# Performance work log

Measured on AMD Instinct MI355X. Metric: run time of the kernel, lower is better.

The kernel has to match this reference:

```python
import jax, jax.numpy as jnp
import numpy as np

N_NODES = 20000
N_EDGES = 320000
N_GRAPHS = 512
IN_FEATS = 128
HID = 256
RDKIT_IN = 2048
RDK_H1, RDK_H2 = 1024, 512
COMB_H1, COMB_H2 = 1024, 512
N_TASKS = 1
EPS = 1e-5


def _lin(k, fan_in, fan_out):
    return jax.random.normal(k, (fan_in, fan_out), jnp.float32) / np.float32(np.sqrt(fan_in))


def setup_inputs() -> dict:
    key = jax.random.key(0)
    ks = jax.random.split(key, 24)
    inp = {}
    inp["node_feats"] = jax.random.normal(ks[0], (N_NODES, IN_FEATS), jnp.float32)
    inp["rdkit_feats"] = jax.random.normal(ks[1], (N_GRAPHS, RDKIT_IN), jnp.float32)
    inp["src"] = jax.random.randint(ks[2], (N_EDGES,), 0, N_NODES, dtype=jnp.int32)
    inp["dst"] = jax.random.randint(ks[3], (N_EDGES,), 0, N_NODES, dtype=jnp.int32)
    # sorted graph ids; first N_GRAPHS entries guarantee every graph has >=1 node
    gid = jnp.concatenate([jnp.arange(N_GRAPHS, dtype=jnp.int32),
                           jax.random.randint(ks[4], (N_NODES - N_GRAPHS,), 0, N_GRAPHS, dtype=jnp.int32)])
    inp["node_gid"] = jnp.sort(gid)
    # GCN layer params (GraphConv W,b + residual Linear + BatchNorm gamma/beta)
    dims = [(IN_FEATS, HID), (HID, HID)]
    for i, (fi, fo) in enumerate(dims, start=1):
        inp[f"W{i}"] = _lin(ks[4 + 4 * i], fi, fo)
        inp[f"b{i}"] = jnp.zeros((fo,), jnp.float32)
        inp[f"rW{i}"] = _lin(ks[5 + 4 * i], fi, fo)
        inp[f"rb{i}"] = jnp.zeros((fo,), jnp.float32)
        inp[f"g{i}"] = jnp.ones((fo,), jnp.float32)
        inp[f"be{i}"] = jnp.zeros((fo,), jnp.float32)
    inp["aw_W"] = _lin(ks[16], HID, 1)
    inp["aw_b"] = jnp.zeros((1,), jnp.float32)
    inp["rk_W1"] = _lin(ks[17], RDKIT_IN, RDK_H1)
    inp["rk_b1"] = jnp.zeros((RDK_H1,), jnp.float32)
    inp["rk_W2"] = _lin(ks[18], RDK_H1, RDK_H2)
    inp["rk_b2"] = jnp.zeros((RDK_H2,), jnp.float32)
    comb_in = RDK_H2 + 2 * HID
    inp["c_W1"] = _lin(ks[19], comb_in, COMB_H1)
    inp["c_b1"] = jnp.zeros((COMB_H1,), jnp.float32)
    inp["c_W2"] = _lin(ks[20], COMB_H1, COMB_H2)
    inp["c_b2"] = jnp.zeros((COMB_H2,), jnp.float32)
    inp["c_W3"] = _lin(ks[21], COMB_H2, N_TASKS)
    inp["c_b3"] = jnp.zeros((N_TASKS,), jnp.float32)
    return inp


def _gcn_layer(h, src, dst, W, b, rW, rb, g, be):
    # GraphConv, norm='none': sum incoming messages of (X W), then bias + relu
    m = h @ W                                                    # [N, out]
    agg = jax.ops.segment_sum(m[src], dst, num_segments=h.shape[0])
    new = jax.nn.relu(agg + b)
    # residual Linear with activation (dgllife GCNLayer)
    new = new + jax.nn.relu(h @ rW + rb)
    # BatchNorm1d over nodes (training-mode batch stats; dropout in eval = identity)
    mu = new.mean(axis=0)
    var = new.var(axis=0)
    return g * (new - mu) * jax.lax.rsqrt(var + EPS) + be


def reference(node_feats, rdkit_feats, src, dst, node_gid,
              W1, b1, rW1, rb1, g1, be1,
              W2, b2, rW2, rb2, g2, be2,
              aw_W, aw_b, rk_W1, rk_b1, rk_W2, rk_b2,
              c_W1, c_b1, c_W2, c_b2, c_W3, c_b3):
    h = _gcn_layer(node_feats, src, dst, W1, b1, rW1, rb1, g1, be1)
    h = _gcn_layer(h, src, dst, W2, b2, rW2, rb2, g2, be2)
    # WeightedSumAndMax readout
    w = jax.nn.sigmoid(h @ aw_W + aw_b)                          # [N, 1]
    hg_sum = jax.ops.segment_sum(h * w, node_gid, num_segments=N_GRAPHS)
    hg_max = jax.ops.segment_max(h, node_gid, num_segments=N_GRAPHS)
    graph_feats = jnp.concatenate([hg_sum, hg_max], axis=1)       # [B, 2*HID]
    # RDKit encoder MLP
    r = jax.nn.relu(rdkit_feats @ rk_W1 + rk_b1)
    r = jax.nn.relu(r @ rk_W2 + rk_b2)
    z = jnp.concatenate([graph_feats, r], axis=1)
    z = jax.nn.relu(z @ c_W1 + c_b1)
    z = jax.nn.relu(z @ c_W2 + c_b2)
    return z @ c_W3 + c_b3                                       # [B, n_tasks]
```

## Files before the change

kernel.cpp:

```cpp
#include <hip/hip_runtime.h>
#include <hip/hip_bf16.h>
#include <cstdint>
#include <cstddef>

#define N_NODES 20000
#define N_EDGES 320000
#define N_GRAPHS 512
#define IN_FEATS 128
#define HID 256

typedef __bf16 bhalf;
typedef __bf16 bhalf8 __attribute__((ext_vector_type(8)));
typedef __bf16 bhalf4 __attribute__((ext_vector_type(4)));
typedef __bf16 bhalf2 __attribute__((ext_vector_type(2)));
typedef float f32x4 __attribute__((ext_vector_type(4)));

template<int RELU, int OUTBF16>
__global__ __launch_bounds__(256) void gemm_mfma(const bhalf* __restrict__ A,
                                                 const bhalf* __restrict__ Bt,
                                                 void* __restrict__ Cv,
                                                 const float* __restrict__ bias,
                                                 int M, int K, int ldc)
{
    __shared__ bhalf As[64 * 64];
    __shared__ bhalf Bs[64 * 64];

    const int t = threadIdx.x;
    const int lane = t & 63, wid = t >> 6;
    const int wm0 = (wid >> 1) * 32, wn0 = (wid & 1) * 32;
    const int m0 = blockIdx.y * 64, n0 = blockIdx.x * 64;
    const int S = gridDim.z, kz = blockIdx.z;
    const int Ks = K / S;

    const int srow = t >> 2;
    const int sc0 = (t & 3) << 3;

    f32x4 acc[2][2] = {};
    uint4 ra0, ra1, rb0, rb1;

    const bool mok = (m0 + srow) < M;
    const bhalf* Abase = A + (size_t)(m0 + srow) * K + (size_t)kz * Ks;
    const bhalf* Bbase = Bt + (size_t)(n0 + srow) * K + (size_t)kz * Ks;

    ra0 = mok ? *(const uint4*)(Abase + sc0)      : make_uint4(0u,0u,0u,0u);
    ra1 = mok ? *(const uint4*)(Abase + sc0 + 32) : make_uint4(0u,0u,0u,0u);
    rb0 = *(const uint4*)(Bbase + sc0);
    rb1 = *(const uint4*)(Bbase + sc0 + 32);

    const int swz = (srow & 7) << 3;
    for (int k0 = 0; k0 < Ks; k0 += 64) {
        __syncthreads();
        *(uint4*)&As[srow * 64 + (sc0 ^ swz)]        = ra0;
        *(uint4*)&As[srow * 64 + ((sc0 + 32) ^ swz)] = ra1;
        *(uint4*)&Bs[srow * 64 + (sc0 ^ swz)]        = rb0;
        *(uint4*)&Bs[srow * 64 + ((sc0 + 32) ^ swz)] = rb1;
        __syncthreads();
        if (k0 + 64 < Ks) {
            const bhalf* An = Abase + k0 + 64;
            const bhalf* Bn = Bbase + k0 + 64;
            ra0 = mok ? *(const uint4*)(An + sc0)      : make_uint4(0u,0u,0u,0u);
            ra1 = mok ? *(const uint4*)(An + sc0 + 32) : make_uint4(0u,0u,0u,0u);
            rb0 = *(const uint4*)(Bn + sc0);
            rb1 = *(const uint4*)(Bn + sc0 + 32);
        }
#pragma unroll
        for (int kb = 0; kb < 2; ++kb) {
            const int kc = kb * 32 + (lane >> 4) * 8;
            bhalf8 af[2], bfr[2];
#pragma unroll
            for (int i = 0; i < 2; ++i) {
                int rA = wm0 + i * 16 + (lane & 15);
                af[i] = *(const bhalf8*)&As[rA * 64 + (kc ^ ((rA & 7) << 3))];
                int rB = wn0 + i * 16 + (lane & 15);
                bfr[i] = *(const bhalf8*)&Bs[rB * 64 + (kc ^ ((rB & 7) << 3))];
            }
#pragma unroll
            for (int mi = 0; mi < 2; ++mi)
#pragma unroll
                for (int ni = 0; ni < 2; ++ni)
                    acc[mi][ni] = __builtin_amdgcn_mfma_f32_16x16x32_bf16(
                        af[mi], bfr[ni], acc[mi][ni], 0, 0, 0);
        }
    }

#pragma unroll
    for (int mi = 0; mi < 2; ++mi)
#pragma unroll
        for (int ni = 0; ni < 2; ++ni) {
            int col = n0 + wn0 + ni * 16 + (lane & 15);
            f32x4 v = acc[mi][ni];
            if (S > 1) {
#pragma unroll
                for (int r = 0; r < 4; ++r) {
                    int row = m0 + wm0 + mi * 16 + (lane >> 4) * 4 + r;
                    if (row < M)
                        ((float*)Cv)[((size_t)kz * M + row) * ldc + col] = v[r];
                }
            } else {
                float bb = bias ? bias[col] : 0.f;
#pragma unroll
                for (int r = 0; r < 4; ++r) {
                    int row = m0 + wm0 + mi * 16 + (lane >> 4) * 4 + r;
                    if (row < M) {
                        float x = v[r] + bb;
                        if (RELU) x = fmaxf(x, 0.f);
                        if (OUTBF16) ((bhalf*)Cv)[(size_t)row * ldc + col] = (bhalf)x;
                        else         ((float*)Cv)[(size_t)row * ldc + col] = x;
                    }
                }
            }
        }
}

__global__ __launch_bounds__(256) void gcn_gemm_fused(const bhalf* __restrict__ Aagg,
                                                      const bhalf* __restrict__ Ax,
                                                      const bhalf* __restrict__ BW,
                                                      const bhalf* __restrict__ BrW,
                                                      const float* __restrict__ b,
                                                      const float* __restrict__ rb,
                                                      bhalf* __restrict__ vout,
                                                      float* __restrict__ stats,
                                                      int M, int K)
{
    __shared__ bhalf As[64 * 64];
    __shared__ bhalf Bs[64 * 64];
    __shared__ float ssum[64], ssq[64];

    const int t = threadIdx.x;
    const int lane = t & 63, wid = t >> 6;
    const int wm0 = (wid >> 1) * 32, wn0 = (wid & 1) * 32;
    const int m0 = blockIdx.y * 64, n0 = blockIdx.x * 64;

    const int srow = t >> 2;
    const int sc0 = (t & 3) << 3;
    const int nk = K >> 6;

    f32x4 accM[2][2] = {};
    f32x4 accR[2][2] = {};
    uint4 ra0, ra1, rb0, rb1;

    const bool mok = (m0 + srow) < M;
    const bhalf* A0r = Aagg + (size_t)(m0 + srow) * K;
    const bhalf* A1r = Ax + (size_t)(m0 + srow) * K;
    const bhalf* B0r = BW + (size_t)(n0 + srow) * K;
    const bhalf* B1r = BrW + (size_t)(n0 + srow) * K;

    ra0 = mok ? *(const uint4*)(A0r + sc0)      : make_uint4(0u,0u,0u,0u);
    ra1 = mok ? *(const uint4*)(A0r + sc0 + 32) : make_uint4(0u,0u,0u,0u);
    rb0 = *(const uint4*)(B0r + sc0);
    rb1 = *(const uint4*)(B0r + sc0 + 32);

    const int swz = (srow & 7) << 3;
    const int total = 2 * nk;
    for (int ii = 0; ii < total; ++ii) {
        __syncthreads();
        *(uint4*)&As[srow * 64 + (sc0 ^ swz)]        = ra0;
        *(uint4*)&As[srow * 64 + ((sc0 + 32) ^ swz)] = ra1;
        *(uint4*)&Bs[srow * 64 + (sc0 ^ swz)]        = rb0;
        *(uint4*)&Bs[srow * 64 + ((sc0 + 32) ^ swz)] = rb1;
        __syncthreads();
        int jj = ii + 1;
        if (jj < total) {
            bool seln = jj >= nk;
            int kk = (seln ? jj - nk : jj) << 6;
            const bhalf* Ab = (seln ? A1r : A0r) + kk;
            const bhalf* Bb = (seln ? B1r : B0r) + kk;
            ra0 = mok ? *(const uint4*)(Ab + sc0)      : make_uint4(0u,0u,0u,0u);
            ra1 = mok ? *(const uint4*)(Ab + sc0 + 32) : make_uint4(0u,0u,0u,0u);
            rb0 = *(const uint4*)(Bb + sc0);
            rb1 = *(const uint4*)(Bb + sc0 + 32);
        }
        const bool selc = ii >= nk;
#pragma unroll
        for (int kb = 0; kb < 2; ++kb) {
            const int kc = kb * 32 + (lane >> 4) * 8;
            bhalf8 af[2], bfr[2];
#pragma unroll
            for (int i = 0; i < 2; ++i) {
                int rA = wm0 + i * 16 + (lane & 15);
                af[i] = *(const bhalf8*)&As[rA * 64 + (kc ^ ((rA & 7) << 3))];
                int rB = wn0 + i * 16 + (lane & 15);
                bfr[i] = *(const bhalf8*)&Bs[rB * 64 + (kc ^ ((rB & 7) << 3))];
            }
            if (!selc) {
#pragma unroll
                for (int mi = 0; mi < 2; ++mi)
#pragma unroll
                    for (int ni = 0; ni < 2; ++ni)
                        accM[mi][ni] = __builtin_amdgcn_mfma_f32_16x16x32_bf16(
                            af[mi], bfr[ni], accM[mi][ni], 0, 0, 0);
            } else {
#pragma unroll
                for (int mi = 0; mi < 2; ++mi)
#pragma unroll
                    for (int ni = 0; ni < 2; ++ni)
                        accR[mi][ni] = __builtin_amdgcn_mfma_f32_16x16x32_bf16(
                            af[mi], bfr[ni], accR[mi][ni], 0, 0, 0);
            }
        }
    }

    if (t < 64) { ssum[t] = 0.f; ssq[t] = 0.f; }
    __syncthreads();
    float sloc[2] = {0.f, 0.f}, s2loc[2] = {0.f, 0.f};
#pragma unroll
    for (int ni = 0; ni < 2; ++ni) {
        int cl = wn0 + ni * 16 + (lane & 15);
        int c = n0 + cl;
        float bb = b[c], rbb = rb[c];
#pragma unroll
        for (int mi = 0; mi < 2; ++mi) {
            f32x4 a0v = accM[mi][ni], a1v = accR[mi][ni];
#pragma unroll
            for (int r = 0; r < 4; ++r) {
                int row = m0 + wm0 + mi * 16 + (lane >> 4) * 4 + r;
                if (row < M) {
                    float x = fmaxf(a0v[r] + bb, 0.f) + fmaxf(a1v[r] + rbb, 0.f);
                    vout[(size_t)row * HID + c] = (bhalf)x;
                    sloc[ni] += x;
                    s2loc[ni] += x * x;
                }
            }
        }
        atomicAdd(&ssum[cl], sloc[ni]);
        atomicAdd(&ssq[cl], s2loc[ni]);
    }
    __syncthreads();
    if (t < 64) {
        atomicAdd(&stats[n0 + t], ssum[t]);
        atomicAdd(&stats[HID + n0 + t], ssq[t]);
    }
}

template<int RELU, int OUTBF16>
__global__ __launch_bounds__(256) void splitk_combine(const float* __restrict__ part,
                                                      int S, int M, int N, int ldo,
                                                      const float* __restrict__ bias,
                                                      void* __restrict__ outv)
{
    int i = blockIdx.x * blockDim.x + threadIdx.x;
    int n4 = N >> 2;
    if (i >= M * n4) return;
    int row = i / n4, c4 = (i - row * n4) << 2;
    float4 s = make_float4(0.f, 0.f, 0.f, 0.f);
    for (int z = 0; z < S; ++z) {
        float4 p = *(const float4*)(part + ((size_t)z * M + row) * N + c4);
        s.x += p.x; s.y += p.y; s.z += p.z; s.w += p.w;
    }
    float4 bb = *(const float4*)(bias + c4);
    s.x += bb.x; s.y += bb.y; s.z += bb.z; s.w += bb.w;
    if (RELU) {
        s.x = fmaxf(s.x, 0.f); s.y = fmaxf(s.y, 0.f);
        s.z = fmaxf(s.z, 0.f); s.w = fmaxf(s.w, 0.f);
    }
    if (OUTBF16) {
        bhalf4 o = {(bhalf)s.x, (bhalf)s.y, (bhalf)s.z, (bhalf)s.w};
        *(bhalf4*)((bhalf*)outv + (size_t)row * ldo + c4) = o;
    } else {
        *(float4*)((float*)outv + (size_t)row * ldo + c4) = s;
    }
}

__global__ __launch_bounds__(128) void splitk_combine_dot(const float* __restrict__ part,
                                                          int S, int M, int N,
                                                          const float* __restrict__ bias,
                                                          const float* __restrict__ W3,
                                                          const float* __restrict__ b3,
                                                          float* __restrict__ out)
{
    int row = blockIdx.x, t = threadIdx.x;
    int c4 = t << 2;
    float4 s = make_float4(0.f, 0.f, 0.f, 0.f);
    for (int z = 0; z < S; ++z) {
        float4 p = *(const float4*)(part + ((size_t)z * M + row) * N + c4);
        s.x += p.x; s.y += p.y; s.z += p.z; s.w += p.w;
    }
    float4 bb = *(const float4*)(bias + c4);
    float4 w = *(const float4*)(W3 + c4);
    float d = fmaxf(s.x + bb.x, 0.f) * w.x + fmaxf(s.y + bb.y, 0.f) * w.y
            + fmaxf(s.z + bb.z, 0.f) * w.z + fmaxf(s.w + bb.w, 0.f) * w.w;
#pragma unroll
    for (int off = 32; off > 0; off >>= 1) d += __shfl_xor(d, off);
    __shared__ float ws2[2];
    if ((t & 63) == 0) ws2[t >> 6] = d;
    __syncthreads();
    if (t == 0) out[row] = ws2[0] + ws2[1] + b3[0];
}

struct WEnt { const float* src; bhalf* dst; int K; int N; int tiles_end; };
struct PrepTab {
    WEnt e[8];
    const float* ca; bhalf* coa; int n4a;
    const float* cb; bhalf* cob; int n4b;
    uint4* zbase; int zn;
};

#define WTILES 4288
#define CONVB  3524

__global__ __launch_bounds__(256) void prep_batch(PrepTab tab)
{
    __shared__ float tile[32][33];
    int tb = blockIdx.x;
    int t = threadIdx.x;
    if (tb < WTILES) {
        int idx = 0;
#pragma unroll
        for (int i = 0; i < 8; ++i)
            if (tb >= tab.e[i].tiles_end) idx = i + 1;
        const WEnt& E = tab.e[idx];
        int t0 = idx ? tab.e[idx - 1].tiles_end : 0;
        int lt = tb - t0;
        int tX = E.N >> 5;
        int bx = (lt % tX) << 5;
        int by = (lt / tX) << 5;
        int tx = t & 31, ty = t >> 5;
#pragma unroll
        for (int i = 0; i < 32; i += 8)
            tile[ty + i][tx] = E.src[(size_t)(by + ty + i) * E.N + bx + tx];
        __syncthreads();
#pragma unroll
        for (int i = 0; i < 32; i += 8)
            E.dst[(size_t)(bx + ty + i) * E.K + by + tx] = (bhalf)tile[tx][ty + i];
    } else if (tb < WTILES + CONVB) {
        int i = (tb - WTILES) * 256 + t;
        const float* s; bhalf* d; int j;
        if (i < tab.n4a) { s = tab.ca; d = tab.coa; j = i; }
        else { j = i - tab.n4a; if (j >= tab.n4b) return; s = tab.cb; d = tab.cob; }
        float4 v = ((const float4*)s)[j];
        bhalf4 o = {(bhalf)v.x, (bhalf)v.y, (bhalf)v.z, (bhalf)v.w};
        ((bhalf4*)d)[j] = o;
    } else {
        int j = (tb - WTILES - CONVB) * 256 + t;
        if (j < tab.zn) tab.zbase[j] = make_uint4(0u, 0u, 0u, 0u);
    }
}

__global__ void csr_count(const int* __restrict__ dst, int* __restrict__ counts)
{
    int e = blockIdx.x * blockDim.x + threadIdx.x;
    if (e >= N_EDGES) return;
    atomicAdd(&counts[dst[e]], 1);
}

__global__ __launch_bounds__(256) void csr_scan_a(const int* __restrict__ counts,
                                                  int* __restrict__ bsum)
{
    int i = blockIdx.x * 256 + threadIdx.x;
    int v = (i < N_NODES) ? counts[i] : 0;
#pragma unroll
    for (int off = 32; off > 0; off >>= 1) v += __shfl_down(v, off);
    __shared__ int ws[4];
    if ((threadIdx.x & 63) == 0) ws[threadIdx.x >> 6] = v;
    __syncthreads();
    if (threadIdx.x == 0) bsum[blockIdx.x] = ws[0] + ws[1] + ws[2] + ws[3];
}

__global__ __launch_bounds__(256) void csr_scan_c(const int* __restrict__ counts,
                                                  const int* __restrict__ bsum, int nb,
                                                  int* __restrict__ offsets)
{
    int t = threadIdx.x, b = blockIdx.x;
    int i = b * 256 + t;
    int v = (i < N_NODES) ? counts[i] : 0;
    int x = v;
#pragma unroll
    for (int off = 1; off < 64; off <<= 1) {
        int y = __shfl_up(x, off);
        if ((t & 63) >= off) x += y;
    }
    __shared__ int wsum[4];
    __shared__ int tmp[128];
    __shared__ int addsh;
    if ((t & 63) == 63) wsum[t >> 6] = x;
    if (t < 128) tmp[t] = (t < nb) ? bsum[t] : 0;
    __syncthreads();
    if (t == 0) {
        int a = 0;
        for (int j = 0; j < b; ++j) a += tmp[j];
        addsh = a;
    }
    __syncthreads();
    int add = addsh;
    for (int w = 0; w < (t >> 6); ++w) add += wsum[w];
    int excl = x - v + add;
    if (i < N_NODES) offsets[i] = excl;
    if (i == N_NODES - 1) offsets[N_NODES] = excl + v;
}

__global__ void csr_fill(const int* __restrict__ src, const int* __restrict__ dst,
                         const int* __restrict__ offsets, int* __restrict__ cursor,
                         int* __restrict__ eidx)
{
    int e = blockIdx.x * blockDim.x + threadIdx.x;
    if (e >= N_EDGES) return;
    int d = dst[e];
    int slot = offsets[d] + atomicAdd(&cursor[d], 1);
    eidx[slot] = src[e];
}

__global__ void csr_sort_wave(const int* __restrict__ offsets, int* __restrict__ eidx)
{
    int gidx = blockIdx.x * blockDim.x + threadIdx.x;
    int n = gidx >> 6, lane = gidx & 63;
    if (n >= N_NODES) return;
    int lo = offsets[n], hi = offsets[n + 1];
    int cnt = hi - lo;
    if (cnt <= 1) return;
    if (cnt <= 64) {
        int v = (lane < cnt) ? eidx[lo + lane] : 0x7fffffff;
        int rank = 0;
        for (int j = 0; j < cnt; ++j) {
            int vj = __shfl(v, j);
            if (vj < v || (vj == v && j < lane)) ++rank;
        }
        if (lane < cnt) eidx[lo + rank] = v;
    } else if (lane == 0) {
        for (int i = lo + 1; i < hi; ++i) {
            int v = eidx[i]; int j = i - 1;
            while (j >= lo && eidx[j] > v) { eidx[j + 1] = eidx[j]; --j; }
            eidx[j + 1] = v;
        }
    }
}

__global__ __launch_bounds__(256) void edge_gather1(const bhalf* __restrict__ m,
                                                    const int* __restrict__ offsets,
                                                    const int* __restrict__ eidx,
                                                    bhalf* __restrict__ agg)
{
    int gidx = blockIdx.x * blockDim.x + threadIdx.x;
    int n = gidx >> 6, lane = gidx & 63;
    if (n >= N_NODES) return;
    int lo = offsets[n], hi = offsets[n + 1];
    const bhalf* base = m + lane * 2;
    float ax = 0.f, ay = 0.f;
    int i = lo;
    for (; i + 4 <= hi; i += 4) {
        bhalf2 v0 = *(const bhalf2*)(base + (size_t)eidx[i] * IN_FEATS);
        bhalf2 v1 = *(const bhalf2*)(base + (size_t)eidx[i + 1] * IN_FEATS);
        bhalf2 v2 = *(const bhalf2*)(base + (size_t)eidx[i + 2] * IN_FEATS);
        bhalf2 v3 = *(const bhalf2*)(base + (size_t)eidx[i + 3] * IN_FEATS);
        ax += ((float)v0.x + (float)v1.x) + ((float)v2.x + (float)v3.x);
        ay += ((float)v0.y + (float)v1.y) + ((float)v2.y + (float)v3.y);
    }
    for (; i < hi; ++i) {
        bhalf2 v0 = *(const bhalf2*)(base + (size_t)eidx[i] * IN_FEATS);
        ax += (float)v0.x; ay += (float)v0.y;
    }
    bhalf2 o = {(bhalf)ax, (bhalf)ay};
    *(bhalf2*)(agg + (size_t)n * IN_FEATS + lane * 2) = o;
}

__global__ __launch_bounds__(256) void edge_gather2(const bhalf* __restrict__ m,
                                                    const int* __restrict__ offsets,
                                                    const int* __restrict__ eidx,
                                                    bhalf* __restrict__ agg)
{
    int gidx = blockIdx.x * blockDim.x + threadIdx.x;
    int w = gidx >> 6, lane = gidx & 63;
    int n = w >> 1, half = w & 1;
    if (n >= N_NODES) return;
    int lo = offsets[n], hi = offsets[n + 1];
    int coff = half * 128 + lane * 2;
    const bhalf* base = m + coff;
    float ax = 0.f, ay = 0.f;
    int i = lo;
    for (; i + 4 <= hi; i += 4) {
        bhalf2 v0 = *(const bhalf2*)(base + (size_t)eidx[i] * HID);
        bhalf2 v1 = *(const bhalf2*)(base + (size_t)eidx[i + 1] * HID);
        bhalf2 v2 = *(const bhalf2*)(base + (size_t)eidx[i + 2] * HID);
        bhalf2 v3 = *(const bhalf2*)(base + (size_t)eidx[i + 3] * HID);
        ax += ((float)v0.x + (float)v1.x) + ((float)v2.x + (float)v3.x);
        ay += ((float)v0.y + (float)v1.y) + ((float)v2.y + (float)v3.y);
    }
    for (; i < hi; ++i) {
        bhalf2 v0 = *(const bhalf2*)(base + (size_t)eidx[i] * HID);
        ax += (float)v0.x; ay += (float)v0.y;
    }
    bhalf2 o = {(bhalf)ax, (bhalf)ay};
    *(bhalf2*)(agg + (size_t)n * HID + coff) = o;
}

template<int MODE>
__global__ __launch_bounds__(256) void bn_row(const bhalf* __restrict__ v,
                                              const float* __restrict__ stats,
                                              float inv_n,
                                              const float* __restrict__ g,
                                              const float* __restrict__ be,
                                              bhalf* __restrict__ outb,
                                              const float* __restrict__ awW,
                                              const float* __restrict__ awb,
                                              float* __restrict__ w)
{
    int gidx = blockIdx.x * blockDim.x + threadIdx.x;
    int n = gidx >> 6, lane = gidx & 63;
    if (n >= N_NODES) return;
    int col = lane * 4;
    bhalf4 vv = *(const bhalf4*)(v + (size_t)n * HID + col);
    float4 sm = *(const float4*)(stats + col);
    float4 sq = *(const float4*)(stats + HID + col);
    float4 gg = *(const float4*)(g + col);
    float4 bb = *(const float4*)(be + col);
    float mux = sm.x * inv_n, muy = sm.y * inv_n, muz = sm.z * inv_n, muw = sm.w * inv_n;
    float rsx = rsqrtf(sq.x * inv_n - mux * mux + 1e-5f);
    float rsy = rsqrtf(sq.y * inv_n - muy * muy + 1e-5f);
    float rsz = rsqrtf(sq.z * inv_n - muz * muz + 1e-5f);
    float rsw = rsqrtf(sq.w * inv_n - muw * muw + 1e-5f);
    float4 o;
    o.x = gg.x * ((float)vv.x - mux) * rsx + bb.x;
    o.y = gg.y * ((float)vv.y - muy) * rsy + bb.y;
    o.z = gg.z * ((float)vv.z - muz) * rsz + bb.z;
    o.w = gg.w * ((float)vv.w - muw) * rsw + bb.w;
    bhalf4 ob = {(bhalf)o.x, (bhalf)o.y, (bhalf)o.z, (bhalf)o.w};
    *(bhalf4*)(outb + (size_t)n * HID + col) = ob;
    if (MODE == 1) {
        float4 wv = *(const float4*)(awW + col);
        float d = o.x * wv.x + o.y * wv.y + o.z * wv.z + o.w * wv.w;
#pragma unroll
        for (int off = 32; off > 0; off >>= 1) d += __shfl_xor(d, off);
        if (lane == 0) w[n] = 1.f / (1.f + expf(-(d + awb[0])));
    }
}

__global__ __launch_bounds__(256) void readout(const bhalf* __restrict__ h,
                                               const float* __restrict__ w,
                                               const int* __restrict__ gid,
                                               bhalf* __restrict__ z)
{
    int g = blockIdx.x, col = threadIdx.x;
    int lo = 0, hi = N_NODES;
    while (lo < hi) { int mid = (lo + hi) >> 1; if (gid[mid] < g) lo = mid + 1; else hi = mid; }
    int start = lo;
    hi = N_NODES;
    while (lo < hi) { int mid = (lo + hi) >> 1; if (gid[mid] <= g) lo = mid + 1; else hi = mid; }
    int end = lo;
    float s = 0.f, mx = -INFINITY;
    for (int n = start; n < end; ++n) {
        float v = (float)h[(size_t)n * HID + col];
        s = fmaf(v, w[n], s);
        mx = fmaxf(mx, v);
    }
    z[(size_t)g * 1024 + col] = (bhalf)s;
    z[(size_t)g * 1024 + HID + col] = (bhalf)mx;
}

extern "C" void kernel_launch(void* const* d_in, const int* in_sizes, int n_in,
                              void* d_out, int out_size, void* d_ws, size_t ws_size,
                              hipStream_t stream)
{
    (void)in_sizes; (void)n_in; (void)out_size; (void)ws_size;

    const float* node_feats = (const float*)d_in[0];
    const float* rdkit      = (const float*)d_in[1];
    const int*   src        = (const int*)d_in[2];
    const int*   dst        = (const int*)d_in[3];
    const int*   gid        = (const int*)d_in[4];
    const float* W1  = (const float*)d_in[5];
    const float* b1  = (const float*)d_in[6];
    const float* rW1 = (const float*)d_in[7];
    const float* rb1 = (const float*)d_in[8];
    const float* g1  = (const float*)d_in[9];
    const float* be1 = (const float*)d_in[10];
    const float* W2  = (const float*)d_in[11];
    const float* b2  = (const float*)d_in[12];
    const float* rW2 = (const float*)d_in[13];
    const float* rb2 = (const float*)d_in[14];
    const float* g2  = (const float*)d_in[15];
    const float* be2 = (const float*)d_in[16];
    const float* aw_W  = (const float*)d_in[17];
    const float* aw_b  = (const float*)d_in[18];
    const float* rk_W1 = (const float*)d_in[19];
    const float* rk_b1 = (const float*)d_in[20];
    const float* rk_W2 = (const float*)d_in[21];
    const float* rk_b2 = (const float*)d_in[22];
    const float* c_W1  = (const float*)d_in[23];
    const float* c_b1  = (const float*)d_in[24];
    const float* c_W2  = (const float*)d_in[25];
    const float* c_b2  = (const float*)d_in[26];
    const float* c_W3  = (const float*)d_in[27];
    const float* c_b3  = (const float*)d_in[28];

    float* out = (float*)d_out;

    const size_t NODE = (size_t)N_NODES * HID;
    bhalf* nfb   = (bhalf*)d_ws;
    bhalf* h1b   = nfb + (size_t)N_NODES * IN_FEATS;
    bhalf* h2b   = h1b + NODE;
    bhalf* aggb  = h2b + NODE;
    bhalf* vb    = aggb + NODE;
    bhalf* W1cat = vb + NODE;
    bhalf* W2cat = W1cat + 512 * 128;
    bhalf* rkW1t = W2cat + 512 * 256;
    bhalf* rkW2t = rkW1t + 2048 * 1024;
    bhalf* cW1t  = rkW2t + 1024 * 512;
    bhalf* cW2t  = cW1t + 1024 * 1024;
    bhalf* rdkb  = cW2t + 1024 * 512;
    float* stats1 = (float*)(rdkb + 512 * 2048);
    float* stats2 = stats1 + 512;
    int*   counts = (int*)(stats2 + 512);
    int*   cursor = counts + N_NODES;
    float* wbuf   = (float*)(cursor + N_NODES);
    int*   offsets = (int*)(wbuf + N_NODES);
    int*   eidx    = offsets + N_NODES + 1;
    int*   bsum    = eidx + N_EDGES;
    bhalf* rkhb  = (bhalf*)(bsum + 128);
    bhalf* zb    = rkhb + 512 * 1024;
    bhalf* ch1b  = zb + 512 * 1024;
    float* spart = (float*)(ch1b + 512 * 1024);

    dim3 blk(256);
    const int EPB = (N_EDGES + 255) / 256;
    const int NPB = (N_NODES + 255) / 256;
    const int NWAVE = (N_NODES * 64) / 256;
    const int NWAVE2 = (N_NODES * 128) / 256;
    dim3 gfused(HID / 64, (N_NODES + 63) / 64);

    PrepTab tab;
    tab.e[0] = {W1,    W1cat,             128, 256,   32};
    tab.e[1] = {rW1,   W1cat + 256 * 128, 128, 256,   64};
    tab.e[2] = {W2,    W2cat,             256, 256,  128};
    tab.e[3] = {rW2,   W2cat + 256 * 256, 256, 256,  192};
    tab.e[4] = {rk_W1, rkW1t,            2048, 1024, 2240};
    tab.e[5] = {rk_W2, rkW2t,            1024, 512,  2752};
    tab.e[6] = {c_W1,  cW1t,             1024, 1024, 3776};
    tab.e[7] = {c_W2,  cW2t,             1024, 512,  4288};
    tab.ca = node_feats; tab.coa = nfb;  tab.n4a = N_NODES * IN_FEATS / 4;
    tab.cb = rdkit;      tab.cob = rdkb; tab.n4b = 512 * 2048 / 4;
    tab.zbase = (uint4*)stats1;
    tab.zn = (1024 + 2 * N_NODES) / 4;
    const int ZB = (tab.zn + 255) / 256;
    prep_batch<<<WTILES + CONVB + ZB, blk, 0, stream>>>(tab);

    csr_count<<<EPB, blk, 0, stream>>>(dst, counts);
    csr_scan_a<<<NPB, blk, 0, stream>>>(counts, bsum);
    csr_scan_c<<<NPB, blk, 0, stream>>>(counts, bsum, NPB, offsets);
    csr_fill<<<EPB, blk, 0, stream>>>(src, dst, offsets, cursor, eidx);
    csr_sort_wave<<<NWAVE, blk, 0, stream>>>(offsets, eidx);

    edge_gather1<<<NWAVE, blk, 0, stream>>>(nfb, offsets, eidx, aggb);
    gcn_gemm_fused<<<gfused, blk, 0, stream>>>(aggb, nfb, W1cat, W1cat + 256 * 128,
                                               b1, rb1, vb, stats1, N_NODES, IN_FEATS);
    bn_row<0><<<NWAVE, blk, 0, stream>>>(vb, stats1, 1.0f / N_NODES, g1, be1,
                                         h1b, nullptr, nullptr, nullptr);

    edge_gather2<<<NWAVE2, blk, 0, stream>>>(h1b, offsets, eidx, aggb);
    gcn_gemm_fused<<<gfused, blk, 0, stream>>>(aggb, h1b, W2cat, W2cat + 256 * 256,
                                               b2, rb2, vb, stats2, N_NODES, HID);
    bn_row<1><<<NWAVE, blk, 0, stream>>>(vb, stats2, 1.0f / N_NODES, g2, be2,
                                         h2b, aw_W, aw_b, wbuf);

    readout<<<N_GRAPHS, HID, 0, stream>>>(h2b, wbuf, gid, zb);

    gemm_mfma<0,0><<<dim3(16, 8, 8), blk, 0, stream>>>(rdkb, rkW1t, spart, nullptr,
                                                       512, 2048, 1024);
    splitk_combine<1,1><<<512, blk, 0, stream>>>(spart, 8, 512, 1024, 1024, rk_b1, rkhb);
    gemm_mfma<0,0><<<dim3(8, 8, 8), blk, 0, stream>>>(rkhb, rkW2t, spart, nullptr,
                                                      512, 1024, 512);
    splitk_combine<1,1><<<256, blk, 0, stream>>>(spart, 8, 512, 512, 1024, rk_b2, zb + 512);

    gemm_mfma<0,0><<<dim3(16, 8, 4), blk, 0, stream>>>(zb, cW1t, spart, nullptr,
                                                       512, 1024, 1024);
    splitk_combine<1,1><<<512, blk, 0, stream>>>(spart, 4, 512, 1024, 1024, c_b1, ch1b);
    gemm_mfma<0,0><<<dim3(8, 8, 8), blk, 0, stream>>>(ch1b, cW2t, spart, nullptr,
                                                      512, 1024, 512);
    splitk_combine_dot<<<512, 128, 0, stream>>>(spart, 8, 512, 512, c_b2, c_W3, c_b3, out);
}
```

Before: 249.5 us.

## Vectorize edge gathers with 16-byte loads and add XCD-aware block swizzle for GEMMs

Both edge-gather kernels now have each lane load 8 bf16 values at once and split a wave into sub-groups that handle different edges in parallel, then combine the partial sums with cross-lane shuffles. Layer 2 now uses one wave per node instead of two, which halves its grid. The GEMM kernels also remap block indices so that neighbouring tiles land on the same XCD, aiming at better L2 reuse. The wider loads should cut the number of memory instructions, at the cost of shuffle reductions and lower utilisation on low-degree nodes.

New measurement: 233.0 us. 1.07x faster.

```diff
diff --git a/kernel.cpp b/kernel.cpp
--- a/kernel.cpp
+++ b/kernel.cpp
@@ -14,6 +14,16 @@
 typedef __bf16 bhalf4 __attribute__((ext_vector_type(4)));
 typedef __bf16 bhalf2 __attribute__((ext_vector_type(2)));
 typedef float f32x4 __attribute__((ext_vector_type(4)));
+
+__device__ __forceinline__ int2 xcd_swz(int bx, int by, int nbx, int nby)
+{
+    int lid = by * nbx + bx;
+    int nwg = nbx * nby;
+    int q = nwg >> 3, r = nwg & 7;
+    int xcd = lid & 7, loc = lid >> 3;
+    int s = (xcd < r ? xcd * (q + 1) : r * (q + 1) + (xcd - r) * q) + loc;
+    return make_int2(s % nbx, s / nbx);
+}
 
 template<int RELU, int OUTBF16>
 __global__ __launch_bounds__(256) void gemm_mfma(const bhalf* __restrict__ A,
@@ -28,7 +38,8 @@
     const int t = threadIdx.x;
     const int lane = t & 63, wid = t >> 6;
     const int wm0 = (wid >> 1) * 32, wn0 = (wid & 1) * 32;
-    const int m0 = blockIdx.y * 64, n0 = blockIdx.x * 64;
+    int2 bsw = xcd_swz(blockIdx.x, blockIdx.y, gridDim.x, gridDim.y);
+    const int m0 = bsw.y * 64, n0 = bsw.x * 64;
     const int S = gridDim.z, kz = blockIdx.z;
     const int Ks = K / S;
 
@@ -129,7 +140,8 @@
     const int t = threadIdx.x;
     const int lane = t & 63, wid = t >> 6;
     const int wm0 = (wid >> 1) * 32, wn0 = (wid & 1) * 32;
-    const int m0 = blockIdx.y * 64, n0 = blockIdx.x * 64;
+    int2 bsw = xcd_swz(blockIdx.x, blockIdx.y, gridDim.x, gridDim.y);
+    const int m0 = bsw.y * 64, n0 = bsw.x * 64;
 
     const int srow = t >> 2;
     const int sc0 = (t & 3) << 3;
@@ -433,23 +445,38 @@
     int n = gidx >> 6, lane = gidx & 63;
     if (n >= N_NODES) return;
     int lo = offsets[n], hi = offsets[n + 1];
-    const bhalf* base = m + lane * 2;
-    float ax = 0.f, ay = 0.f;
+    int sub = lane >> 4;
+    int colb = (lane & 15) * 8;
+    float acc[8] = {};
     int i = lo;
-    for (; i + 4 <= hi; i += 4) {
-        bhalf2 v0 = *(const bhalf2*)(base + (size_t)eidx[i] * IN_FEATS);
-        bhalf2 v1 = *(const bhalf2*)(base + (size_t)eidx[i + 1] * IN_FEATS);
-        bhalf2 v2 = *(const bhalf2*)(base + (size_t)eidx[i + 2] * IN_FEATS);
-        bhalf2 v3 = *(const bhalf2*)(base + (size_t)eidx[i + 3] * IN_FEATS);
-        ax += ((float)v0.x + (float)v1.x) + ((float)v2.x + (float)v3.x);
-        ay += ((float)v0.y + (float)v1.y) + ((float)v2.y + (float)v3.y);
-    }
-    for (; i < hi; ++i) {
-        bhalf2 v0 = *(const bhalf2*)(base + (size_t)eidx[i] * IN_FEATS);
-        ax += (float)v0.x; ay += (float)v0.y;
-    }
-    bhalf2 o = {(bhalf)ax, (bhalf)ay};
-    *(bhalf2*)(agg + (size_t)n * IN_FEATS + lane * 2) = o;
+    for (; i + 8 <= hi; i += 8) {
+        bhalf8 v0 = *(const bhalf8*)(m + (size_t)eidx[i + sub] * IN_FEATS + colb);
+        bhalf8 v1 = *(const bhalf8*)(m + (size_t)eidx[i + 4 + sub] * IN_FEATS + colb);
+#pragma unroll
+        for (int j = 0; j < 8; ++j) acc[j] += (float)v0[j] + (float)v1[j];
+    }
+    if (i + 4 <= hi) {
+        bhalf8 v0 = *(const bhalf8*)(m + (size_t)eidx[i + sub] * IN_FEATS + colb);
+#pragma unroll
+        for (int j = 0; j < 8; ++j) acc[j] += (float)v0[j];
+        i += 4;
+    }
+    if (i < hi && sub < hi - i) {
+        bhalf8 v0 = *(const bhalf8*)(m + (size_t)eidx[i + sub] * IN_FEATS + colb);
+#pragma unroll
+        for (int j = 0; j < 8; ++j) acc[j] += (float)v0[j];
+    }
+#pragma unroll
+    for (int j = 0; j < 8; ++j) {
+        acc[j] += __shfl_xor(acc[j], 16);
+        acc[j] += __shfl_xor(acc[j], 32);
+    }
+    if (sub == 0) {
+        bhalf8 o;
+#pragma unroll
+        for (int j = 0; j < 8; ++j) o[j] = (bhalf)acc[j];
+        *(bhalf8*)(agg + (size_t)n * IN_FEATS + colb) = o;
+    }
 }
 
 __global__ __launch_bounds__(256) void edge_gather2(const bhalf* __restrict__ m,
@@ -458,28 +485,41 @@
                                                     bhalf* __restrict__ agg)
 {
     int gidx = blockIdx.x * blockDim.x + threadIdx.x;
-    int w = gidx >> 6, lane = gidx & 63;
-    int n = w >> 1, half = w & 1;
+    int n = gidx >> 6, lane = gidx & 63;
     if (n >= N_NODES) return;
     int lo = offsets[n], hi = offsets[n + 1];
-    int coff = half * 128 + lane * 2;
-    const bhalf* base = m + coff;
-    float ax = 0.f, ay = 0.f;
+    int sub = lane >> 5;
+    int colb = (lane & 31) * 8;
+    float acc[8] = {};
     int i = lo;
-    for (; i + 4 <= hi; i += 4) {
-        bhalf2 v0 = *(const bhalf2*)(base + (size_t)eidx[i] * HID);
-        bhalf2 v1 = *(const bhalf2*)(base + (size_t)eidx[i + 1] * HID);
-        bhalf2 v2 = *(const bhalf2*)(base + (size_t)eidx[i + 2] * HID);
-        bhalf2 v3 = *(const bhalf2*)(base + (size_t)eidx[i + 3] * HID);
-        ax += ((float)v0.x + (float)v1.x) + ((float)v2.x + (float)v3.x);
-        ay += ((float)v0.y + (float)v1.y) + ((float)v2.y + (float)v3.y);
-    }
-    for (; i < hi; ++i) {
-        bhalf2 v0 = *(const bhalf2*)(base + (size_t)eidx[i] * HID);
-        ax += (float)v0.x; ay += (float)v0.y;
-    }
-    bhalf2 o = {(bhalf)ax, (bhalf)ay};
-    *(bhalf2*)(agg + (size_t)n * HID + coff) = o;
+    for (; i + 8 <= hi; i += 8) {
+        bhalf8 v0 = *(const bhalf8*)(m + (size_t)eidx[i + sub] * HID + colb);
+        bhalf8 v1 = *(const bhalf8*)(m + (size_t)eidx[i + 2 + sub] * HID + colb);
+        bhalf8 v2 = *(const bhalf8*)(m + (size_t)eidx[i + 4 + sub] * HID + colb);
+        bhalf8 v3 = *(const bhalf8*)(m + (size_t)eidx[i + 6 + sub] * HID + colb);
+#pragma unroll
+        for (int j = 0; j < 8; ++j)
+            acc[j] += ((float)v0[j] + (float)v1[j]) + ((float)v2[j] + (float)v3[j]);
+    }
+    for (; i + 2 <= hi; i += 2) {
+        bhalf8 v0 = *(const bhalf8*)(m + (size_t)eidx[i + sub] * HID + colb);
+#pragma unroll
+        for (int j = 0; j < 8; ++j) acc[j] += (float)v0[j];
+    }
+    if (i < hi && sub == 0) {
+        bhalf8 v0 = *(const bhalf8*)(m + (size_t)eidx[i] * HID + colb);
+#pragma unroll
+        for (int j = 0; j < 8; ++j) acc[j] += (float)v0[j];
+    }
+#pragma unroll
+    for (int j = 0; j < 8; ++j)
+        acc[j] += __shfl_xor(acc[j], 32);
+    if (sub == 0) {
+        bhalf8 o;
+#pragma unroll
+        for (int j = 0; j < 8; ++j) o[j] = (bhalf)acc[j];
+        *(bhalf8*)(agg + (size_t)n * HID + colb) = o;
+    }
 }
 
 template<int MODE>
@@ -613,7 +653,6 @@
     const int EPB = (N_EDGES + 255) / 256;
     const int NPB = (N_NODES + 255) / 256;
     const int NWAVE = (N_NODES * 64) / 256;
-    const int NWAVE2 = (N_NODES * 128) / 256;
     dim3 gfused(HID / 64, (N_NODES + 63) / 64);
 
     PrepTab tab;
@@ -644,7 +683,7 @@
     bn_row<0><<<NWAVE, blk, 0, stream>>>(vb, stats1, 1.0f / N_NODES, g1, be1,
                                          h1b, nullptr, nullptr, nullptr);
 
-    edge_gather2<<<NWAVE2, blk, 0, stream>>>(h1b, offsets, eidx, aggb);
+    edge_gather2<<<NWAVE, blk, 0, stream>>>(h1b, offsets, eidx, aggb);
     gcn_gemm_fused<<<gfused, blk, 0, stream>>>(aggb, h1b, W2cat, W2cat + 256 * 256,
                                                b2, rb2, vb, stats2, N_NODES, HID);
     bn_row<1><<<NWAVE, blk, 0, stream>>>(vb, stats2, 1.0f / N_NODES, g2, be2,
```
